# Optimization experiments

Measured on AMD Instinct MI355X. Metric: run time of the kernel, lower is better.

## Reference

```python
import jax, jax.numpy as jnp
import numpy as np

B, S, D = 2, 2048, 1024
H, HD, R = 16, 64, 128
BLOCK, TOPK = 64, 4
ROPE_BASE = 100000.0
NEG = -1e30  # finite large-negative instead of -inf to avoid NaN rows


def _rope_tables(seq_len, dim, dtype):
    inv_freq = 1.0 / (ROPE_BASE ** (jnp.arange(0, dim, 2, dtype=jnp.float32) / dim))
    freqs = jnp.arange(seq_len, dtype=jnp.float32)[:, None] * inv_freq[None, :]  # [S, dim/2]
    emb = jnp.concatenate([freqs, freqs], axis=-1)  # [S, dim]
    return jnp.cos(emb).astype(dtype), jnp.sin(emb).astype(dtype)


def _rotate_half(t):
    t1, t2 = jnp.split(t, 2, axis=-1)
    return jnp.concatenate([-t2, t1], axis=-1)


def _apply_rope(t, cos, sin):
    # t: [B, H, S, HD]; cos/sin: [S, HD]
    return t * cos[None, None] + _rotate_half(t) * sin[None, None]


def setup_inputs() -> dict:
    key = jax.random.key(0)
    ks = jax.random.split(key, 6)
    s = 0.02
    return {
        "x": jax.random.normal(ks[0], (B, S, D), jnp.float32),
        "w_q": jax.random.normal(ks[1], (D, D), jnp.float32) * s,
        "w_kv_down": jax.random.normal(ks[2], (R, D), jnp.float32) * s,
        "w_kv_up": jax.random.normal(ks[3], (2 * D, R), jnp.float32) * s,
        "w_out": jax.random.normal(ks[4], (D, D), jnp.float32) * s,
        "w_scorer": jax.random.normal(ks[5], (1, D), jnp.float32) * s,
    }


def reference(x, w_q, w_kv_down, w_kv_up, w_out, w_scorer):
    b, s, d = x.shape
    nb = s // BLOCK  # S divisible by block_size here

    q = (x @ w_q.T).reshape(b, s, H, HD).transpose(0, 2, 1, 3)  # [B,H,S,HD]
    latent = x @ w_kv_down.T                                      # [B,S,R]
    kv = latent @ w_kv_up.T                                       # [B,S,2D]
    k, v = jnp.split(kv, 2, axis=-1)
    k = k.reshape(b, s, H, HD).transpose(0, 2, 1, 3)
    v = v.reshape(b, s, H, HD).transpose(0, 2, 1, 3)

    cos, sin = _rope_tables(s, HD, x.dtype)
    q = _apply_rope(q, cos, sin)
    k = _apply_rope(k, cos, sin)

    # block relevance scores from mean-pooled block reps of x
    block_reps = x.reshape(b, nb, BLOCK, d).mean(axis=2)          # [B,nb,D]
    block_scores = (block_reps @ w_scorer.T)[..., 0]              # [B,nb]
    _, top_idx = jax.lax.top_k(block_scores, min(TOPK, nb))       # [B,topk]

    # sparse key mask: True where key position lies in a selected block
    sel = jnp.zeros((b, nb), dtype=bool)
    sel = sel.at[jnp.arange(b)[:, None], top_idx].set(True)       # [B,nb]
    sparse_mask = jnp.repeat(sel, BLOCK, axis=1)                  # [B,S]

    causal = jnp.tril(jnp.ones((s, s), dtype=bool))               # True = allowed
    allowed = sparse_mask[:, None, None, :] & causal[None, None]  # [B,1,S,S]

    scale = 1.0 / jnp.sqrt(jnp.asarray(HD, x.dtype))
    scores = jnp.einsum("bhqd,bhkd->bhqk", q, k) * scale          # [B,H,S,S]
    scores = jnp.where(allowed, scores, NEG)
    attn = jax.nn.softmax(scores, axis=-1)
    out = jnp.einsum("bhqk,bhkd->bhqd", attn, v)                  # [B,H,S,HD]
    out = out.transpose(0, 2, 1, 3).reshape(b, s, d)
    return out @ w_out.T
```

## Files before the change

kernel.cpp:

```cpp
#include <hip/hip_runtime.h>
#include <hip/hip_bf16.h>
#include <math.h>

#define B_ 2
#define S_ 2048
#define D_ 1024
#define H_ 16
#define HD_ 64
#define R_ 128
#define NBLK 32
#define TOPK_ 4
#define BS_ (B_*S_)

typedef __attribute__((ext_vector_type(8))) short bf16x8;
typedef __attribute__((ext_vector_type(4))) float f32x4;

__device__ __forceinline__ unsigned short f2bf(float f) {
    unsigned int u = __float_as_uint(f);
    u += 0x7fffu + ((u >> 16) & 1u);
    return (unsigned short)(u >> 16);
}
__device__ __forceinline__ float bf2f(unsigned short h) {
    return __uint_as_float(((unsigned int)h) << 16);
}
__device__ __forceinline__ unsigned int pack2(float a, float b) {
    return (unsigned int)f2bf(a) | ((unsigned int)f2bf(b) << 16);
}
__device__ __forceinline__ void gload_lds16(const void* g, void* l) {
    __builtin_amdgcn_global_load_lds((const __attribute__((address_space(1))) void*)g,
                                     (__attribute__((address_space(3))) void*)l, 16, 0, 0);
}

__global__ void rope_tables_k(float* __restrict__ cosT, float* __restrict__ sinT) {
    int idx = blockIdx.x*256 + threadIdx.x;
    if (idx >= S_*HD_) return;
    int s  = idx >> 6;
    int hd = idx & 63;
    int j = (hd < 32) ? hd : hd - 32;
    float inv = powf(100000.0f, -((float)(2*j) / 64.0f));
    float fr = (float)s * inv;
    cosT[idx] = cosf(fr);
    sinT[idx] = sinf(fr);
}

__global__ __launch_bounds__(256) void cvtw_k(const float* __restrict__ wq,
        const float* __restrict__ wkd, const float* __restrict__ wku,
        const float* __restrict__ wo, unsigned short* __restrict__ wcat,
        unsigned short* __restrict__ wkub, unsigned short* __restrict__ wob) {
    const int blk = blockIdx.x;
    const float* src; unsigned short* dst; int base;
    if      (blk < 512) { src = wq;  dst = wcat;            base = blk;       }
    else if (blk < 576) { src = wkd; dst = wcat + 1048576;  base = blk - 512; }
    else if (blk < 704) { src = wku; dst = wkub;            base = blk - 576; }
    else                { src = wo;  dst = wob;             base = blk - 704; }
    const int i = base*2048 + threadIdx.x*8;
    float4 a = *(const float4*)&src[i];
    float4 b = *(const float4*)&src[i+4];
    uint4 o;
    o.x = pack2(a.x, a.y); o.y = pack2(a.z, a.w);
    o.z = pack2(b.x, b.y); o.w = pack2(b.z, b.w);
    *(uint4*)&dst[i] = o;
}

template<int EPI>
__global__ __launch_bounds__(256) void gemm_mfma_k(const unsigned short* __restrict__ A,
        const unsigned short* __restrict__ Bm, int M, int N, int K,
        void* __restrict__ o0, void* __restrict__ o1,
        const float* __restrict__ cosT, const float* __restrict__ sinT,
        float* __restrict__ vsum) {
    __shared__ unsigned short shbuf[128*64 + 64*64];
    unsigned short* As = shbuf;
    unsigned short* Bs = shbuf + 128*64;
    const int tid  = threadIdx.x;
    const int wave = tid >> 6, lane = tid & 63;
    const int bm = blockIdx.y << 7, bn = blockIdx.x << 6;
    const int g  = lane >> 4, qc = lane & 15;
    const int srow  = lane >> 3;
    const int sslot = (lane & 7) ^ srow;

    f32x4 acc[2][4];
    #pragma unroll
    for (int m=0;m<2;m++)
        #pragma unroll
        for (int n=0;n<4;n++)
            acc[m][n] = (f32x4){0.f,0.f,0.f,0.f};

    for (int k0 = 0; k0 < K; k0 += 64) {
        __syncthreads();
        #pragma unroll
        for (int it = 0; it < 4; ++it) {
            const int chunk = (it << 2) | wave;
            const int row   = (chunk << 3) | srow;
            gload_lds16(A + (size_t)(bm + row) * K + k0 + (sslot << 3), &As[chunk << 9]);
        }
        #pragma unroll
        for (int it = 0; it < 2; ++it) {
            const int chunk = (it << 2) | wave;
            const int row   = (chunk << 3) | srow;
            gload_lds16(Bm + (size_t)(bn + row) * K + k0 + (sslot << 3), &Bs[chunk << 9]);
        }
        __syncthreads();
        #pragma unroll
        for (int ks = 0; ks < 2; ++ks) {
            const int swb = ((ks << 2) | g) ^ (lane & 7);
            bf16x8 af[2], bfr[4];
            #pragma unroll
            for (int m = 0; m < 2; ++m)
                af[m]  = *(const bf16x8*)&As[(((wave << 5) + (m << 4) + qc) << 6) + (swb << 3)];
            #pragma unroll
            for (int n = 0; n < 4; ++n)
                bfr[n] = *(const bf16x8*)&Bs[(((n << 4) + qc) << 6) + (swb << 3)];
            #pragma unroll
            for (int m = 0; m < 2; ++m)
                #pragma unroll
                for (int n = 0; n < 4; ++n)
                    acc[m][n] = __builtin_amdgcn_mfma_f32_16x16x32_bf16(af[m], bfr[n], acc[m][n], 0, 0, 0);
        }
    }

    if (EPI == 0) {
        float* C = (float*)o0;
        #pragma unroll
        for (int m = 0; m < 2; ++m) {
            const int r0 = bm + (wave << 5) + (m << 4) + (g << 2);
            #pragma unroll
            for (int n = 0; n < 4; ++n) {
                const int c = bn + (n << 4) + qc;
                #pragma unroll
                for (int j = 0; j < 4; ++j)
                    C[(size_t)(r0 + j) * N + c] = acc[m][n][j];
            }
        }
    } else {
        const bool isrope = (bn < 1024);
        if (isrope) {
            const int h = bn >> 6;
            unsigned short* dst = (unsigned short*)o0;
            #pragma unroll
            for (int m = 0; m < 2; ++m) {
                const int r0 = bm + (wave << 5) + (m << 4) + (g << 2);
                #pragma unroll
                for (int j = 0; j < 4; ++j) {
                    const int row = r0 + j;
                    const int b = row >> 11, s = row & (S_-1);
                    const size_t obase = ((size_t)(b*H_ + h) * S_ + s) << 6;
                    #pragma unroll
                    for (int n = 0; n < 4; ++n) {
                        const int hd = (n << 4) + qc;
                        const float c_ = cosT[(s << 6) + hd];
                        const float sn = sinT[(s << 6) + hd];
                        const float rot = (n < 2) ? -acc[m][n ^ 2][j] : acc[m][n ^ 2][j];
                        dst[obase + hd] = f2bf(acc[m][n][j] * c_ + rot * sn);
                    }
                }
            }
        } else if (EPI == 1) {
            unsigned short* latb = (unsigned short*)o1;
            const int c0 = bn - 1024;
            #pragma unroll
            for (int m = 0; m < 2; ++m) {
                const int r0 = bm + (wave << 5) + (m << 4) + (g << 2);
                #pragma unroll
                for (int n = 0; n < 4; ++n) {
                    const int c = c0 + (n << 4) + qc;
                    #pragma unroll
                    for (int j = 0; j < 4; ++j)
                        latb[(size_t)(r0 + j) * R_ + c] = f2bf(acc[m][n][j]);
                }
            }
        } else {
            const int h  = (bn >> 6) - 16;
            const int b  = bm >> 11, s0 = bm & (S_-1);
            const int bh = (b << 4) + h;
            unsigned short* vtb = (unsigned short*)o1;
            unsigned short (*T)[72] = (unsigned short(*)[72])shbuf;
            __syncthreads();
            #pragma unroll
            for (int m = 0; m < 2; ++m) {
                const int r0 = (wave << 5) + (m << 4) + (g << 2);
                #pragma unroll
                for (int n = 0; n < 4; ++n)
                    #pragma unroll
                    for (int j = 0; j < 4; ++j)
                        T[r0 + j][(n << 4) + qc] = f2bf(acc[m][n][j]);
            }
            __syncthreads();
            #pragma unroll
            for (int u = 0; u < 2; ++u) {
                const int kb = (s0 >> 6) + u;
                unsigned short* dst = vtb + (((size_t)(bh * NBLK + kb)) << 12);
                #pragma unroll
                for (int uu = 0; uu < 2; ++uu) {
                    const int idx = (uu << 8) + tid;
                    const int dd = idx >> 3, k0 = (idx & 7) << 3;
                    unsigned short tmp[8];
                    float sm = 0.f;
                    #pragma unroll
                    for (int j = 0; j < 8; ++j) { tmp[j] = T[(u << 6) + k0 + j][dd]; sm += bf2f(tmp[j]); }
                    *(uint4*)&dst[(size_t)(dd << 6) + k0] = *(uint4*)tmp;
                    sm += __shfl_xor(sm, 1);
                    sm += __shfl_xor(sm, 2);
                    sm += __shfl_xor(sm, 4);
                    if ((tid & 7) == 0) atomicAdd(&vsum[(bh << 6) + dd], sm);
                }
            }
        }
    }
}

__global__ __launch_bounds__(256) void rowscore_cvt_k(const float* __restrict__ x,
        const float* __restrict__ wsc, float* __restrict__ rows,
        unsigned short* __restrict__ xb) {
    const int wid  = (blockIdx.x << 2) + (threadIdx.x >> 6);
    const int lane = threadIdx.x & 63;
    #pragma unroll
    for (int r = 0; r < 4; ++r) {
        const int row = (wid << 2) + r;
        const float* xp = x + (size_t)row * D_;
        unsigned short* xo = xb + (size_t)row * D_;
        float acc = 0.f;
        #pragma unroll
        for (int j = 0; j < 4; ++j) {
            const int off = ((j << 6) + lane) << 2;
            float4 xv = *(const float4*)&xp[off];
            float4 wv = *(const float4*)&wsc[off];
            acc = fmaf(xv.x, wv.x, acc);
            acc = fmaf(xv.y, wv.y, acc);
            acc = fmaf(xv.z, wv.z, acc);
            acc = fmaf(xv.w, wv.w, acc);
            uint2 o; o.x = pack2(xv.x, xv.y); o.y = pack2(xv.z, xv.w);
            *(uint2*)&xo[off] = o;
        }
        #pragma unroll
        for (int m = 1; m <= 32; m <<= 1) acc += __shfl_xor(acc, m);
        if (lane == 0) rows[row] = acc;
    }
}

__global__ __launch_bounds__(256) void blocktopk_k(const float* __restrict__ rows,
        int* __restrict__ sel) {
    __shared__ float bs[64];
    const int bk = threadIdx.x >> 2, qt = threadIdx.x & 3;
    const float* rp = rows + (bk << 6) + (qt << 4);
    float p = 0.f;
    #pragma unroll
    for (int i = 0; i < 16; ++i) p += rp[i];
    p += __shfl_xor(p, 1);
    p += __shfl_xor(p, 2);
    if (qt == 0) bs[bk] = p;
    __syncthreads();
    if (threadIdx.x < B_) {
        const int b = threadIdx.x;
        float sc[NBLK];
        for (int i = 0; i < NBLK; ++i) sc[i] = bs[b * NBLK + i];
        for (int j = 0; j < TOPK_; ++j) {
            float best = -INFINITY; int bi = 0;
            for (int i = 0; i < NBLK; ++i)
                if (sc[i] > best) { best = sc[i]; bi = i; }
            sel[b * TOPK_ + j] = bi;
            sc[bi] = -INFINITY;
        }
    }
}

__global__ __launch_bounds__(256) void attn_mfma_k(const unsigned short* __restrict__ qrb,
        const unsigned short* __restrict__ krb, const unsigned short* __restrict__ vtb,
        const int* __restrict__ sel, const float* __restrict__ vsum,
        unsigned short* __restrict__ attno) {
    const int qb = blockIdx.x & (NBLK-1);
    const int bh = blockIdx.x >> 5;
    const int b  = bh >> 4;
    const int h  = bh & 15;
    const int tid  = threadIdx.x;
    const int wave = tid >> 6, lane = tid & 63;
    const int g = lane >> 4, qc = lane & 15;

    __shared__ unsigned short Pl[4][16][72];
    __shared__ float cfl[4][16];
    __shared__ float lvl[4][16];

    int selb[4];
    #pragma unroll
    for (int j=0;j<4;j++) selb[j] = sel[(b<<2)+j];
    const bool diag = (selb[0]==qb)|(selb[1]==qb)|(selb[2]==qb)|(selb[3]==qb);

    const unsigned short* qp = qrb + (((size_t)bh*S_ + (qb<<6) + (wave<<4) + qc) << 6);
    bf16x8 bq[2];
    bq[0] = *(const bf16x8*)(qp + (g<<3));
    bq[1] = *(const bf16x8*)(qp + 32 + (g<<3));

    f32x4 oacc[4];
    #pragma unroll
    for (int n=0;n<4;n++) oacc[n] = (f32x4){0.f,0.f,0.f,0.f};
    float mrun = -INFINITY, lrun = 0.f;
    int nproc = 0;
    const int qib = (wave<<4) + qc;

    for (int j = 0; j < 5; ++j) {
        int kb; bool isdiag;
        if (j < 4) { kb = selb[j]; isdiag = false; if (kb >= qb) continue; }
        else       { if (!diag) continue; kb = qb; isdiag = true; }
        nproc++;
        const unsigned short* kB = krb + (((size_t)bh*S_ + (kb<<6)) << 6);
        const unsigned short* vT = vtb + (((size_t)(bh*NBLK + kb)) << 12);

        bf16x8 ak[2][4], vb[2][4];
        #pragma unroll
        for (int ks=0;ks<2;ks++)
            #pragma unroll
            for (int m=0;m<4;m++)
                ak[ks][m] = *(const bf16x8*)(kB + (((m<<4)+qc)<<6) + (ks<<5) + (g<<3));
        #pragma unroll
        for (int ks=0;ks<2;ks++)
            #pragma unroll
            for (int n=0;n<4;n++)
                vb[ks][n] = *(const bf16x8*)(vT + (((n<<4)+qc)<<6) + (ks<<5) + (g<<3));

        f32x4 sf[4];
        #pragma unroll
        for (int m=0;m<4;m++) sf[m] = (f32x4){0.f,0.f,0.f,0.f};
        #pragma unroll
        for (int ks=0;ks<2;ks++)
            #pragma unroll
            for (int m=0;m<4;m++)
                sf[m] = __builtin_amdgcn_mfma_f32_16x16x32_bf16(ak[ks][m], bq[ks], sf[m], 0, 0, 0);

        float s[16];
        float bmax = -INFINITY;
        #pragma unroll
        for (int m=0;m<4;m++)
            #pragma unroll
            for (int r2=0;r2<4;r2++) {
                const int kl = (m<<4)+(g<<2)+r2;
                float v = sf[m][r2]*0.125f;
                if (isdiag && kl > qib) v = -1e30f;
                s[(m<<2)+r2] = v;
                bmax = fmaxf(bmax, v);
            }
        bmax = fmaxf(bmax, __shfl_xor(bmax, 16));
        bmax = fmaxf(bmax, __shfl_xor(bmax, 32));
        const float mnew = fmaxf(mrun, bmax);
        const float cf = __expf(mrun - mnew);
        float ls = 0.f;
        #pragma unroll
        for (int m=0;m<4;m++) {
            float p0 = __expf(s[(m<<2)+0]-mnew);
            float p1 = __expf(s[(m<<2)+1]-mnew);
            float p2 = __expf(s[(m<<2)+2]-mnew);
            float p3 = __expf(s[(m<<2)+3]-mnew);
            ls += p0+p1+p2+p3;
            const int koff = (m<<4)+(g<<2);
            *(unsigned int*)&Pl[wave][qc][koff]   = pack2(p0,p1);
            *(unsigned int*)&Pl[wave][qc][koff+2] = pack2(p2,p3);
        }
        ls += __shfl_xor(ls, 16);
        ls += __shfl_xor(ls, 32);
        lrun = lrun*cf + ls;
        cfl[wave][qc] = cf;
        f32x4 cf4 = *(const f32x4*)&cfl[wave][g<<2];
        #pragma unroll
        for (int n=0;n<4;n++) oacc[n] *= cf4;
        #pragma unroll
        for (int ks=0;ks<2;ks++) {
            bf16x8 pa = *(const bf16x8*)&Pl[wave][qc][(ks<<5)+(g<<3)];
            #pragma unroll
            for (int n=0;n<4;n++)
                oacc[n] = __builtin_amdgcn_mfma_f32_16x16x32_bf16(pa, vb[ks][n], oacc[n], 0, 0, 0);
        }
        mrun = mnew;
    }

    f32x4 il4 = (f32x4){0.f,0.f,0.f,0.f};
    if (nproc) {
        lvl[wave][qc] = 1.0f / lrun;
        il4 = *(const f32x4*)&lvl[wave][g<<2];
    }
    #pragma unroll
    for (int n=0;n<4;n++)
        #pragma unroll
        for (int r2=0;r2<4;r2++) {
            float val = nproc ? oacc[n][r2]*il4[r2]
                              : vsum[(bh<<6)+(n<<4)+qc] * (1.0f/(float)S_);
            const int row = (qb<<6) + (wave<<4) + (g<<2) + r2;
            attno[(((size_t)(b*S_+row))<<10) + (h<<6) + (n<<4) + qc] = f2bf(val);
        }
}

extern "C" void kernel_launch(void* const* d_in, const int* in_sizes, int n_in,
                              void* d_out, int out_size, void* d_ws, size_t ws_size,
                              hipStream_t stream) {
    (void)in_sizes; (void)n_in; (void)out_size; (void)ws_size;
    const float* x     = (const float*)d_in[0];
    const float* w_q   = (const float*)d_in[1];
    const float* w_kvd = (const float*)d_in[2];
    const float* w_kvu = (const float*)d_in[3];
    const float* w_o   = (const float*)d_in[4];
    const float* w_sc  = (const float*)d_in[5];
    float* out = (float*)d_out;

    char* p = (char*)d_ws;
    auto alloc = [&](size_t bytes) -> void* {
        void* r = (void*)p;
        p += (bytes + 255) & ~(size_t)255;
        return r;
    };
    float* cosT  = (float*)alloc((size_t)S_*HD_*4);
    float* sinT  = (float*)alloc((size_t)S_*HD_*4);
    unsigned short* xb    = (unsigned short*)alloc((size_t)BS_*D_*2);
    unsigned short* wcat  = (unsigned short*)alloc((size_t)(D_+R_)*D_*2);
    unsigned short* wkub  = (unsigned short*)alloc((size_t)2*D_*R_*2);
    unsigned short* wob   = (unsigned short*)alloc((size_t)D_*D_*2);
    unsigned short* latb  = (unsigned short*)alloc((size_t)BS_*R_*2);
    unsigned short* qrb   = (unsigned short*)alloc((size_t)BS_*D_*2);
    unsigned short* krb   = (unsigned short*)alloc((size_t)BS_*D_*2);
    unsigned short* vtb   = (unsigned short*)alloc((size_t)BS_*D_*2);
    unsigned short* attnob= (unsigned short*)alloc((size_t)BS_*D_*2);
    float* rows   = (float*)alloc((size_t)BS_*4);
    int*   sel    = (int*)  alloc((size_t)B_*TOPK_*4);
    float* vsum   = (float*)alloc((size_t)B_*H_*HD_*4);

    rope_tables_k<<<(S_*HD_+255)/256, 256, 0, stream>>>(cosT, sinT);
    cvtw_k<<<1216, 256, 0, stream>>>(w_q, w_kvd, w_kvu, w_o, wcat, wkub, wob);
    rowscore_cvt_k<<<256, 256, 0, stream>>>(x, w_sc, rows, xb);
    blocktopk_k<<<1, 256, 0, stream>>>(rows, sel);

    gemm_mfma_k<1><<<dim3((D_+R_)/64, BS_/128), 256, 0, stream>>>(
        xb, wcat, BS_, D_+R_, D_, qrb, latb, cosT, sinT, nullptr);
    hipMemsetAsync(vsum, 0, (size_t)B_*H_*HD_*4, stream);
    gemm_mfma_k<2><<<dim3(2*D_/64, BS_/128), 256, 0, stream>>>(
        latb, wkub, BS_, 2*D_, R_, krb, vtb, cosT, sinT, vsum);

    attn_mfma_k<<<B_*H_*NBLK, 256, 0, stream>>>(qrb, krb, vtb, sel, vsum, attnob);
    gemm_mfma_k<0><<<dim3(D_/64, BS_/128), 256, 0, stream>>>(
        attnob, wob, BS_, D_, D_, out, nullptr, nullptr, nullptr, nullptr);
}
```

Baseline: 169.3 us.

## Double-buffer GEMM LDS tiles, remap blocks for XCD locality, stage attention K/V in LDS

```diff
diff --git a/kernel.cpp b/kernel.cpp
--- a/kernel.cpp
+++ b/kernel.cpp
@@ -68,12 +68,13 @@
         void* __restrict__ o0, void* __restrict__ o1,
         const float* __restrict__ cosT, const float* __restrict__ sinT,
         float* __restrict__ vsum) {
-    __shared__ unsigned short shbuf[128*64 + 64*64];
-    unsigned short* As = shbuf;
-    unsigned short* Bs = shbuf + 128*64;
+    __shared__ unsigned short shbuf[2][12288];
     const int tid  = threadIdx.x;
     const int wave = tid >> 6, lane = tid & 63;
-    const int bm = blockIdx.y << 7, bn = blockIdx.x << 6;
+    const int nx = N >> 6;
+    const int ob = blockIdx.x;
+    const int w  = ((ob & 7) * (gridDim.x >> 3)) + (ob >> 3);
+    const int bm = (w / nx) << 7, bn = (w % nx) << 6;
     const int g  = lane >> 4, qc = lane & 15;
     const int srow  = lane >> 3;
     const int sslot = (lane & 7) ^ srow;
@@ -85,8 +86,11 @@
         for (int n=0;n<4;n++)
             acc[m][n] = (f32x4){0.f,0.f,0.f,0.f};
 
-    for (int k0 = 0; k0 < K; k0 += 64) {
-        __syncthreads();
+    const int NT = K >> 6;
+    auto STAGE = [&](int buf, int t) {
+        const int k0 = t << 6;
+        unsigned short* As = shbuf[buf];
+        unsigned short* Bs = shbuf[buf] + 8192;
         #pragma unroll
         for (int it = 0; it < 4; ++it) {
             const int chunk = (it << 2) | wave;
@@ -99,7 +103,14 @@
             const int row   = (chunk << 3) | srow;
             gload_lds16(Bm + (size_t)(bn + row) * K + k0 + (sslot << 3), &Bs[chunk << 9]);
         }
-        __syncthreads();
+    };
+
+    STAGE(0, 0);
+    __syncthreads();
+    for (int t = 0; t < NT; ++t) {
+        if (t + 1 < NT) STAGE((t + 1) & 1, t + 1);
+        const unsigned short* As = shbuf[t & 1];
+        const unsigned short* Bs = shbuf[t & 1] + 8192;
         #pragma unroll
         for (int ks = 0; ks < 2; ++ks) {
             const int swb = ((ks << 2) | g) ^ (lane & 7);
@@ -116,6 +127,7 @@
                 for (int n = 0; n < 4; ++n)
                     acc[m][n] = __builtin_amdgcn_mfma_f32_16x16x32_bf16(af[m], bfr[n], acc[m][n], 0, 0, 0);
         }
+        __syncthreads();
     }
 
     if (EPI == 0) {
@@ -173,8 +185,7 @@
             const int b  = bm >> 11, s0 = bm & (S_-1);
             const int bh = (b << 4) + h;
             unsigned short* vtb = (unsigned short*)o1;
-            unsigned short (*T)[72] = (unsigned short(*)[72])shbuf;
-            __syncthreads();
+            unsigned short (*T)[72] = (unsigned short(*)[72])&shbuf[0][0];
             #pragma unroll
             for (int m = 0; m < 2; ++m) {
                 const int r0 = (wave << 5) + (m << 4) + (g << 2);
@@ -275,6 +286,8 @@
     const int wave = tid >> 6, lane = tid & 63;
     const int g = lane >> 4, qc = lane & 15;
 
+    __shared__ unsigned short Ks[64][72];
+    __shared__ unsigned short Vt[64][72];
     __shared__ unsigned short Pl[4][16][72];
     __shared__ float cfl[4][16];
     __shared__ float lvl[4][16];
@@ -301,29 +314,28 @@
         if (j < 4) { kb = selb[j]; isdiag = false; if (kb >= qb) continue; }
         else       { if (!diag) continue; kb = qb; isdiag = true; }
         nproc++;
-        const unsigned short* kB = krb + (((size_t)bh*S_ + (kb<<6)) << 6);
-        const unsigned short* vT = vtb + (((size_t)(bh*NBLK + kb)) << 12);
-
-        bf16x8 ak[2][4], vb[2][4];
+        const uint4* gk = (const uint4*)(krb + (((size_t)bh*S_ + (kb<<6)) << 6));
+        const uint4* gv = (const uint4*)(vtb + (((size_t)(bh*NBLK + kb)) << 12));
+        __syncthreads();
+        #pragma unroll
+        for (int u=0;u<2;u++) {
+            int idx = (u<<8) + tid;
+            int r = idx>>3, c = (idx&7)<<3;
+            *(uint4*)&Ks[r][c] = gk[idx];
+            *(uint4*)&Vt[r][c] = gv[idx];
+        }
+        __syncthreads();
+
+        f32x4 sf[4];
+        #pragma unroll
+        for (int m=0;m<4;m++) sf[m] = (f32x4){0.f,0.f,0.f,0.f};
         #pragma unroll
         for (int ks=0;ks<2;ks++)
             #pragma unroll
-            for (int m=0;m<4;m++)
-                ak[ks][m] = *(const bf16x8*)(kB + (((m<<4)+qc)<<6) + (ks<<5) + (g<<3));
-        #pragma unroll
-        for (int ks=0;ks<2;ks++)
-            #pragma unroll
-            for (int n=0;n<4;n++)
-                vb[ks][n] = *(const bf16x8*)(vT + (((n<<4)+qc)<<6) + (ks<<5) + (g<<3));
-
-        f32x4 sf[4];
-        #pragma unroll
-        for (int m=0;m<4;m++) sf[m] = (f32x4){0.f,0.f,0.f,0.f};
-        #pragma unroll
-        for (int ks=0;ks<2;ks++)
-            #pragma unroll
-            for (int m=0;m<4;m++)
-                sf[m] = __builtin_amdgcn_mfma_f32_16x16x32_bf16(ak[ks][m], bq[ks], sf[m], 0, 0, 0);
+            for (int m=0;m<4;m++) {
+                bf16x8 ak = *(const bf16x8*)&Ks[(m<<4)+qc][(ks<<5)+(g<<3)];
+                sf[m] = __builtin_amdgcn_mfma_f32_16x16x32_bf16(ak, bq[ks], sf[m], 0, 0, 0);
+            }
 
         float s[16];
         float bmax = -INFINITY;
@@ -364,8 +376,10 @@
         for (int ks=0;ks<2;ks++) {
             bf16x8 pa = *(const bf16x8*)&Pl[wave][qc][(ks<<5)+(g<<3)];
             #pragma unroll
-            for (int n=0;n<4;n++)
-                oacc[n] = __builtin_amdgcn_mfma_f32_16x16x32_bf16(pa, vb[ks][n], oacc[n], 0, 0, 0);
+            for (int n=0;n<4;n++) {
+                bf16x8 vb = *(const bf16x8*)&Vt[(n<<4)+qc][(ks<<5)+(g<<3)];
+                oacc[n] = __builtin_amdgcn_mfma_f32_16x16x32_bf16(pa, vb, oacc[n], 0, 0, 0);
+            }
         }
         mrun = mnew;
     }
@@ -424,13 +438,13 @@
     rowscore_cvt_k<<<256, 256, 0, stream>>>(x, w_sc, rows, xb);
     blocktopk_k<<<1, 256, 0, stream>>>(rows, sel);
 
-    gemm_mfma_k<1><<<dim3((D_+R_)/64, BS_/128), 256, 0, stream>>>(
+    gemm_mfma_k<1><<<576, 256, 0, stream>>>(
         xb, wcat, BS_, D_+R_, D_, qrb, latb, cosT, sinT, nullptr);
     hipMemsetAsync(vsum, 0, (size_t)B_*H_*HD_*4, stream);
-    gemm_mfma_k<2><<<dim3(2*D_/64, BS_/128), 256, 0, stream>>>(
+    gemm_mfma_k<2><<<1024, 256, 0, stream>>>(
         latb, wkub, BS_, 2*D_, R_, krb, vtb, cosT, sinT, vsum);
 
     attn_mfma_k<<<B_*H_*NBLK, 256, 0, stream>>>(qrb, krb, vtb, sel, vsum, attnob);
-    gemm_mfma_k<0><<<dim3(D_/64, BS_/128), 256, 0, stream>>>(
+    gemm_mfma_k<0><<<512, 256, 0, stream>>>(
         attnob, wob, BS_, D_, D_, out, nullptr, nullptr, nullptr, nullptr);
 }
```

New measurement: 152.6 us. -9.8%, faster.
